# Kernel tuning notes

Hardware: AMD Instinct MI355X
Metric: run time of the kernel (lower is better)

Reference implementation:

```python
import jax, jax.numpy as jnp
import numpy as np

N_HOPS = 3
VOCAB, D = 100000, 300
B, S, T = 128, 2048, 4
N_CLASSES = 3


def setup_inputs() -> dict:
    key = jax.random.key(0)
    ks = jax.random.split(key, 9)
    return {
        "inputs": jax.random.randint(ks[0], (B, S), 0, VOCAB, dtype=jnp.int64 if jax.config.jax_enable_x64 else jnp.int32),
        "targets": jax.random.randint(ks[1], (B, T), 0, VOCAB, dtype=jnp.int64 if jax.config.jax_enable_x64 else jnp.int32),
        "emb_table": jax.random.normal(ks[2], (VOCAB, D), dtype=jnp.float32) * 0.1,
        "W_att": jax.random.normal(ks[3], (2 * D, 1), dtype=jnp.float32) * 0.05,
        "b_att": jax.random.normal(ks[4], (1,), dtype=jnp.float32) * 0.05,
        "W_tr": jax.random.normal(ks[5], (D, D), dtype=jnp.float32) * 0.05,
        "b_tr": jax.random.normal(ks[6], (D,), dtype=jnp.float32) * 0.05,
        "W_out": jax.random.normal(ks[7], (D, N_CLASSES), dtype=jnp.float32) * 0.05,
        "b_out": jax.random.normal(ks[8], (N_CLASSES,), dtype=jnp.float32) * 0.05,
    }


def reference(inputs, targets, emb_table, W_att, b_att, W_tr, b_tr, W_out, b_out):
    # Embedding lookups (dropout prob = 0.0 -> identity)
    we = emb_table[inputs]    # [B, S, D] word/context embeddings
    te = emb_table[targets]   # [B, T, D] aspect-term embeddings
    d = we.shape[-1]
    # Split concat-linear: cat([we, u]) @ W_att == we @ Wa + u @ Wu (avoids [B,S,2D] intermediate)
    Wa, Wu = W_att[:d], W_att[d:]          # each [D, 1]
    u = jnp.mean(te, axis=1, keepdims=True)  # [B, 1, D]
    for _ in range(N_HOPS):
        g = jnp.tanh(we @ Wa + u @ Wu + b_att)          # [B, S, 1]
        a = jax.nn.softmax(g, axis=1)                    # softmax over sequence
        vec = jnp.einsum('bs,bsd->bd', a[..., 0], we)    # [B, D] attention-weighted sum
        te = vec[:, None, :] + te @ W_tr + b_tr          # [B, T, D] (broadcast add)
        u = jnp.mean(te, axis=1, keepdims=True)          # [B, 1, D]
    return u[:, 0, :] @ W_out + b_out                    # [B, n_classes]
```

## Files before the change

### kernel.cpp

```cpp
#include <hip/hip_runtime.h>
#include <hip/hip_bf16.h>

#define VOCAB 100000
#define D 300
#define B 128
#define S 2048
#define T 4

#define WS_V      0
#define WS_WTWU   3600
#define WS_WT2WU  3900
#define WS_WTWO   4200
#define WS_W2WO   5100
#define WS_WT3WO  6000
#define WS_CONST  6900
#define WS_DSCAL  6916
#define WS_PROJ   7940


__device__ __forceinline__ float wave_red(float x) {
    #pragma unroll
    for (int m = 1; m < 64; m <<= 1) x += __shfl_xor(x, m, 64);
    return x;
}

__global__ __launch_bounds__(64) void k_derive1(const float* __restrict__ Watt,
                                                const float* __restrict__ Wtr,
                                                const float* __restrict__ Wout,
                                                float* __restrict__ ws) {
    int i = blockIdx.x, lane = threadIdx.x;
    const float* wrow = Wtr + (size_t)i * D;
    float au = 0.f, a0 = 0.f, a1 = 0.f, a2 = 0.f;
    for (int j = lane; j < D; j += 64) {
        float w = wrow[j];
        au += w * Watt[D + j];
        a0 += w * Wout[j * 3 + 0];
        a1 += w * Wout[j * 3 + 1];
        a2 += w * Wout[j * 3 + 2];
    }
    au = wave_red(au); a0 = wave_red(a0); a1 = wave_red(a1); a2 = wave_red(a2);
    if (lane == 0) {
        ws[WS_WTWU + i] = au;
        ws[WS_WTWO + i * 3 + 0] = a0;
        ws[WS_WTWO + i * 3 + 1] = a1;
        ws[WS_WTWO + i * 3 + 2] = a2;
    }
}

__global__ __launch_bounds__(64) void k_derive2(const float* __restrict__ Wtr,
                                                float* __restrict__ ws) {
    int i = blockIdx.x, lane = threadIdx.x;
    const float* wrow = Wtr + (size_t)i * D;
    float au = 0.f, a0 = 0.f, a1 = 0.f, a2 = 0.f;
    for (int j = lane; j < D; j += 64) {
        float w = wrow[j];
        au += w * ws[WS_WTWU + j];
        a0 += w * ws[WS_WTWO + j * 3 + 0];
        a1 += w * ws[WS_WTWO + j * 3 + 1];
        a2 += w * ws[WS_WTWO + j * 3 + 2];
    }
    au = wave_red(au); a0 = wave_red(a0); a1 = wave_red(a1); a2 = wave_red(a2);
    if (lane == 0) {
        ws[WS_WT2WU + i] = au;
        ws[WS_W2WO + i * 3 + 0] = a0;
        ws[WS_W2WO + i * 3 + 1] = a1;
        ws[WS_W2WO + i * 3 + 2] = a2;
    }
}

__global__ __launch_bounds__(64) void k_derive3(const float* __restrict__ Watt,
                                                const float* __restrict__ Wtr,
                                                const float* __restrict__ Wout,
                                                float* __restrict__ ws) {
    int i = blockIdx.x, lane = threadIdx.x;
    const float* wrow = Wtr + (size_t)i * D;
    float a0 = 0.f, a1 = 0.f, a2 = 0.f;
    for (int j = lane; j < D; j += 64) {
        float w = wrow[j];
        a0 += w * ws[WS_W2WO + j * 3 + 0];
        a1 += w * ws[WS_W2WO + j * 3 + 1];
        a2 += w * ws[WS_W2WO + j * 3 + 2];
    }
    a0 = wave_red(a0); a1 = wave_red(a1); a2 = wave_red(a2);
    if (lane == 0) {
        ws[WS_WT3WO + i * 3 + 0] = a0;
        ws[WS_WT3WO + i * 3 + 1] = a1;
        ws[WS_WT3WO + i * 3 + 2] = a2;
    }
    if (lane < 12) {
        float val;
        if      (lane == 0) val = Watt[i];
        else if (lane == 1) val = Watt[D + i];
        else if (lane == 2) val = ws[WS_WTWU + i];
        else if (lane < 6)  val = Wout[i * 3 + (lane - 3)];
        else if (lane < 9)  val = ws[WS_WTWO + i * 3 + (lane - 6)];
        else                val = ws[WS_W2WO + i * 3 + (lane - 9)];
        ws[WS_V + i * 12 + lane] = val;
    }
}

__global__ __launch_bounds__(64) void k_small(const int* __restrict__ targets,
                                              const float* __restrict__ E,
                                              const float* __restrict__ Watt,
                                              const float* __restrict__ Wout,
                                              const float* __restrict__ btr,
                                              float* __restrict__ ws) {
    int lane = threadIdx.x;
    if (blockIdx.x < B) {
        int b = blockIdx.x;
        int t0 = targets[b * T + 0], t1 = targets[b * T + 1];
        int t2 = targets[b * T + 2], t3 = targets[b * T + 3];
        const float* r0 = E + (size_t)t0 * D;
        const float* r1 = E + (size_t)t1 * D;
        const float* r2 = E + (size_t)t2 * D;
        const float* r3 = E + (size_t)t3 * D;
        float a0 = 0.f, a1 = 0.f, a2 = 0.f, a3 = 0.f, a4 = 0.f, a5 = 0.f;
        for (int i = lane; i < D; i += 64) {
            float u = 0.25f * (r0[i] + r1[i] + r2[i] + r3[i]);
            a0 += u * Watt[D + i];
            a1 += u * ws[WS_WTWU + i];
            a2 += u * ws[WS_WT2WU + i];
            a3 += u * ws[WS_WT3WO + i * 3 + 0];
            a4 += u * ws[WS_WT3WO + i * 3 + 1];
            a5 += u * ws[WS_WT3WO + i * 3 + 2];
        }
        a0 = wave_red(a0); a1 = wave_red(a1); a2 = wave_red(a2);
        a3 = wave_red(a3); a4 = wave_red(a4); a5 = wave_red(a5);
        if (lane == 0) {
            float* o = ws + WS_DSCAL + b * 8;
            o[0] = a0; o[1] = a1; o[2] = a2; o[3] = a3; o[4] = a4; o[5] = a5;
        }
    } else {
        float acc[11];
        #pragma unroll
        for (int k = 0; k < 11; ++k) acc[k] = 0.f;
        for (int i = lane; i < D; i += 64) {
            float bt = btr[i];
            acc[0] += bt * Watt[D + i];
            acc[1] += bt * ws[WS_WTWU + i];
            acc[2] += bt * Wout[i * 3 + 0];
            acc[3] += bt * Wout[i * 3 + 1];
            acc[4] += bt * Wout[i * 3 + 2];
            acc[5] += bt * ws[WS_WTWO + i * 3 + 0];
            acc[6] += bt * ws[WS_WTWO + i * 3 + 1];
            acc[7] += bt * ws[WS_WTWO + i * 3 + 2];
            acc[8] += bt * ws[WS_W2WO + i * 3 + 0];
            acc[9] += bt * ws[WS_W2WO + i * 3 + 1];
            acc[10] += bt * ws[WS_W2WO + i * 3 + 2];
        }
        #pragma unroll
        for (int k = 0; k < 11; ++k) acc[k] = wave_red(acc[k]);
        if (lane == 0) {
            #pragma unroll
            for (int k = 0; k < 11; ++k) ws[WS_CONST + k] = acc[k];
        }
    }
}

__global__ __launch_bounds__(256) void k_proj(const float* __restrict__ E,
                                              const float* __restrict__ Vg,
                                              float* __restrict__ proj) {
    int lane  = threadIdx.x & 63;
    int wave  = (blockIdx.x * blockDim.x + threadIdx.x) >> 6;
    int nwave = (gridDim.x * blockDim.x) >> 6;

    float v[5][12];
    #pragma unroll
    for (int j = 0; j < 5; ++j) {
        int i = lane + 64 * j;
        if (i < D) {
            const float4* p = (const float4*)(Vg + (size_t)i * 12);
            float4 a = p[0], bb = p[1], cc = p[2];
            v[j][0] = a.x;  v[j][1] = a.y;  v[j][2]  = a.z;  v[j][3]  = a.w;
            v[j][4] = bb.x; v[j][5] = bb.y; v[j][6]  = bb.z; v[j][7]  = bb.w;
            v[j][8] = cc.x; v[j][9] = cc.y; v[j][10] = cc.z; v[j][11] = cc.w;
        } else {
            #pragma unroll
            for (int k = 0; k < 12; ++k) v[j][k] = 0.f;
        }
    }

    for (int row = wave; row < VOCAB; row += nwave) {
        const float* er = E + (size_t)row * D;
        float e[5];
        #pragma unroll
        for (int j = 0; j < 5; ++j) {
            int i = lane + 64 * j;
            e[j] = (i < D) ? er[i] : 0.f;
        }
        float p[12];
        #pragma unroll
        for (int k = 0; k < 12; ++k) p[k] = 0.f;
        #pragma unroll
        for (int j = 0; j < 5; ++j) {
            #pragma unroll
            for (int k = 0; k < 12; ++k) p[k] += e[j] * v[j][k];
        }
        #pragma unroll
        for (int m = 1; m < 64; m <<= 1) {
            #pragma unroll
            for (int k = 0; k < 12; ++k) p[k] += __shfl_xor(p[k], m, 64);
        }
        if (lane == 0) {
            float4* dst = (float4*)(proj + (size_t)row * 12);
            dst[0] = make_float4(p[0], p[1], p[2],  p[3]);
            dst[1] = make_float4(p[4], p[5], p[6],  p[7]);
            dst[2] = make_float4(p[8], p[9], p[10], p[11]);
        }
    }
}

__global__ __launch_bounds__(512) void k_hops(const int* __restrict__ inputs,
                                              const float* __restrict__ ws,
                                              const float* __restrict__ batt,
                                              const float* __restrict__ bout,
                                              float* __restrict__ out) {
    __shared__ float wred[8][13];
    __shared__ float sc[4];
    int b = blockIdx.x, tid = threadIdx.x, wave = tid >> 6, lane = tid & 63;
    const float* proj = ws + WS_PROJ;
    const float* cst  = ws + WS_CONST;
    const float* dsc  = ws + WS_DSCAL + b * 8;
    const int*   inp  = inputs + (size_t)b * S;

    float pv[4][12];
    #pragma unroll
    for (int q = 0; q < 4; ++q) {
        int s = tid + 512 * q;
        int idx = inp[s];
        const float4* pr = (const float4*)(proj + (size_t)idx * 12);
        float4 x = pr[0], y = pr[1], z = pr[2];
        pv[q][0] = x.x; pv[q][1] = x.y; pv[q][2]  = x.z; pv[q][3]  = x.w;
        pv[q][4] = y.x; pv[q][5] = y.y; pv[q][6]  = y.z; pv[q][7]  = y.w;
        pv[q][8] = z.x; pv[q][9] = z.y; pv[q][10] = z.z; pv[q][11] = z.w;
    }

    if (tid == 0) sc[0] = dsc[0] + batt[0];
    __syncthreads();
    float c = sc[0];

    float o3c0 = 0.f, o3c1 = 0.f, o3c2 = 0.f, uWtWu = 0.f;

    #pragma unroll
    for (int hop = 0; hop < 3; ++hop) {
        float acc[12];
        #pragma unroll
        for (int k = 0; k < 12; ++k) acc[k] = 0.f;
        #pragma unroll
        for (int q = 0; q < 4; ++q) {
            float g = tanhf(pv[q][0] + c);
            float e = __expf(g);
            acc[11] += e;
            #pragma unroll
            for (int k = 1; k < 12; ++k) acc[k - 1] += e * pv[q][k];
        }
        #pragma unroll
        for (int m = 1; m < 64; m <<= 1) {
            #pragma unroll
            for (int k = 0; k < 12; ++k) acc[k] += __shfl_xor(acc[k], m, 64);
        }
        if (lane == 0) {
            #pragma unroll
            for (int k = 0; k < 12; ++k) wred[wave][k] = acc[k];
        }
        __syncthreads();
        if (tid == 0) {
            float A[12];
            #pragma unroll
            for (int k = 0; k < 12; ++k) {
                float s = 0.f;
                #pragma unroll
                for (int w = 0; w < 8; ++w) s += wred[w][k];
                A[k] = s;
            }
            float inv = 1.0f / A[11];
            if (hop == 0) {
                o3c0  = A[8] * inv + dsc[3] + cst[8];
                o3c1  = A[9] * inv + dsc[4] + cst[9];
                o3c2  = A[10] * inv + dsc[5] + cst[10];
                uWtWu = A[1] * inv + dsc[2] + cst[1];
                sc[0] = A[0] * inv + dsc[1] + cst[0] + batt[0];
            } else if (hop == 1) {
                o3c0  = A[5] * inv + o3c0 + cst[5];
                o3c1  = A[6] * inv + o3c1 + cst[6];
                o3c2  = A[7] * inv + o3c2 + cst[7];
                sc[0] = A[0] * inv + uWtWu + cst[0] + batt[0];
            } else {
                out[b * 3 + 0] = A[2] * inv + o3c0 + cst[2] + bout[0];
                out[b * 3 + 1] = A[3] * inv + o3c1 + cst[3] + bout[1];
                out[b * 3 + 2] = A[4] * inv + o3c2 + cst[4] + bout[2];
            }
        }
        __syncthreads();
        c = sc[0];
    }
}

extern "C" void kernel_launch(void* const* d_in, const int* in_sizes, int n_in,
                              void* d_out, int out_size, void* d_ws, size_t ws_size,
                              hipStream_t stream) {
    const int*   inputs  = (const int*)  d_in[0];
    const int*   targets = (const int*)  d_in[1];
    const float* emb     = (const float*)d_in[2];
    const float* Watt    = (const float*)d_in[3];
    const float* batt    = (const float*)d_in[4];
    const float* Wtr     = (const float*)d_in[5];
    const float* btr     = (const float*)d_in[6];
    const float* Wout    = (const float*)d_in[7];
    const float* bout    = (const float*)d_in[8];
    float* ws  = (float*)d_ws;
    float* out = (float*)d_out;

    hipLaunchKernelGGL(k_derive1, dim3(D),    dim3(64),  0, stream, Watt, Wtr, Wout, ws);
    hipLaunchKernelGGL(k_derive2, dim3(D),    dim3(64),  0, stream, Wtr, ws);
    hipLaunchKernelGGL(k_derive3, dim3(D),    dim3(64),  0, stream, Watt, Wtr, Wout, ws);
    hipLaunchKernelGGL(k_proj,    dim3(2048), dim3(256), 0, stream, emb, ws + WS_V, ws + WS_PROJ);
    hipLaunchKernelGGL(k_small,   dim3(B + 1), dim3(64), 0, stream, targets, emb, Watt, Wout, btr, ws);
    hipLaunchKernelGGL(k_hops,    dim3(B),    dim3(512), 0, stream, inputs, ws, batt, bout, out);
}
```

Baseline: 255.2 us.

## Assign one vocab row per lane in projection and widen hop blocks to 1024

The vocabulary projection kernel now has each lane compute one full embedding row against the 12 projection vectors with float4 loads, instead of one wave per row followed by a 6-step shuffle reduction for 12 values. This removes the per-row cross-lane reduction cost. The trade-off is that adjacent lanes read rows 1200 bytes apart, so loads are strided rather than coalesced. The hop kernel uses 1024 threads per batch row with fewer sequence elements per thread, and the cross-wave sum is parallelised across 12 threads instead of done serially by thread 0.

New measurement: 235.9 us. 7.6% less time.

```diff
diff --git a/kernel.cpp b/kernel.cpp
--- a/kernel.cpp
+++ b/kernel.cpp
@@ -160,62 +160,42 @@
 __global__ __launch_bounds__(256) void k_proj(const float* __restrict__ E,
                                               const float* __restrict__ Vg,
                                               float* __restrict__ proj) {
-    int lane  = threadIdx.x & 63;
-    int wave  = (blockIdx.x * blockDim.x + threadIdx.x) >> 6;
-    int nwave = (gridDim.x * blockDim.x) >> 6;
-
-    float v[5][12];
-    #pragma unroll
-    for (int j = 0; j < 5; ++j) {
-        int i = lane + 64 * j;
-        if (i < D) {
-            const float4* p = (const float4*)(Vg + (size_t)i * 12);
-            float4 a = p[0], bb = p[1], cc = p[2];
-            v[j][0] = a.x;  v[j][1] = a.y;  v[j][2]  = a.z;  v[j][3]  = a.w;
-            v[j][4] = bb.x; v[j][5] = bb.y; v[j][6]  = bb.z; v[j][7]  = bb.w;
-            v[j][8] = cc.x; v[j][9] = cc.y; v[j][10] = cc.z; v[j][11] = cc.w;
-        } else {
-            #pragma unroll
-            for (int k = 0; k < 12; ++k) v[j][k] = 0.f;
-        }
-    }
-
-    for (int row = wave; row < VOCAB; row += nwave) {
-        const float* er = E + (size_t)row * D;
-        float e[5];
-        #pragma unroll
-        for (int j = 0; j < 5; ++j) {
-            int i = lane + 64 * j;
-            e[j] = (i < D) ? er[i] : 0.f;
-        }
-        float p[12];
-        #pragma unroll
-        for (int k = 0; k < 12; ++k) p[k] = 0.f;
-        #pragma unroll
-        for (int j = 0; j < 5; ++j) {
-            #pragma unroll
-            for (int k = 0; k < 12; ++k) p[k] += e[j] * v[j][k];
-        }
-        #pragma unroll
-        for (int m = 1; m < 64; m <<= 1) {
-            #pragma unroll
-            for (int k = 0; k < 12; ++k) p[k] += __shfl_xor(p[k], m, 64);
-        }
-        if (lane == 0) {
-            float4* dst = (float4*)(proj + (size_t)row * 12);
-            dst[0] = make_float4(p[0], p[1], p[2],  p[3]);
-            dst[1] = make_float4(p[4], p[5], p[6],  p[7]);
-            dst[2] = make_float4(p[8], p[9], p[10], p[11]);
-        }
-    }
-}
-
-__global__ __launch_bounds__(512) void k_hops(const int* __restrict__ inputs,
-                                              const float* __restrict__ ws,
-                                              const float* __restrict__ batt,
-                                              const float* __restrict__ bout,
-                                              float* __restrict__ out) {
-    __shared__ float wred[8][13];
+    int lane = threadIdx.x & 63;
+    int wid  = (blockIdx.x * blockDim.x + threadIdx.x) >> 6;
+    int row  = wid * 64 + lane;
+    if (row >= VOCAB) return;
+
+    const float4* er = (const float4*)(E + (size_t)row * D);
+    float acc[12];
+    #pragma unroll
+    for (int c = 0; c < 12; ++c) acc[c] = 0.f;
+
+    #pragma unroll 5
+    for (int k4 = 0; k4 < 75; ++k4) {
+        float4 e = er[k4];
+        const float* vp = Vg + k4 * 48;
+        #pragma unroll
+        for (int c = 0; c < 12; ++c) {
+            acc[c] += e.x * vp[c];
+            acc[c] += e.y * vp[12 + c];
+            acc[c] += e.z * vp[24 + c];
+            acc[c] += e.w * vp[36 + c];
+        }
+    }
+
+    float4* dst = (float4*)(proj + (size_t)row * 12);
+    dst[0] = make_float4(acc[0], acc[1], acc[2],  acc[3]);
+    dst[1] = make_float4(acc[4], acc[5], acc[6],  acc[7]);
+    dst[2] = make_float4(acc[8], acc[9], acc[10], acc[11]);
+}
+
+__global__ __launch_bounds__(1024) void k_hops(const int* __restrict__ inputs,
+                                               const float* __restrict__ ws,
+                                               const float* __restrict__ batt,
+                                               const float* __restrict__ bout,
+                                               float* __restrict__ out) {
+    __shared__ float wred[16][13];
+    __shared__ float Ash[13];
     __shared__ float sc[4];
     int b = blockIdx.x, tid = threadIdx.x, wave = tid >> 6, lane = tid & 63;
     const float* proj = ws + WS_PROJ;
@@ -223,10 +203,10 @@
     const float* dsc  = ws + WS_DSCAL + b * 8;
     const int*   inp  = inputs + (size_t)b * S;
 
-    float pv[4][12];
-    #pragma unroll
-    for (int q = 0; q < 4; ++q) {
-        int s = tid + 512 * q;
+    float pv[2][12];
+    #pragma unroll
+    for (int q = 0; q < 2; ++q) {
+        int s = tid + 1024 * q;
         int idx = inp[s];
         const float4* pr = (const float4*)(proj + (size_t)idx * 12);
         float4 x = pr[0], y = pr[1], z = pr[2];
@@ -247,7 +227,7 @@
         #pragma unroll
         for (int k = 0; k < 12; ++k) acc[k] = 0.f;
         #pragma unroll
-        for (int q = 0; q < 4; ++q) {
+        for (int q = 0; q < 2; ++q) {
             float g = tanhf(pv[q][0] + c);
             float e = __expf(g);
             acc[11] += e;
@@ -264,31 +244,30 @@
             for (int k = 0; k < 12; ++k) wred[wave][k] = acc[k];
         }
         __syncthreads();
+        if (tid < 12) {
+            float s = 0.f;
+            #pragma unroll
+            for (int w = 0; w < 16; ++w) s += wred[w][tid];
+            Ash[tid] = s;
+        }
+        __syncthreads();
         if (tid == 0) {
-            float A[12];
-            #pragma unroll
-            for (int k = 0; k < 12; ++k) {
-                float s = 0.f;
-                #pragma unroll
-                for (int w = 0; w < 8; ++w) s += wred[w][k];
-                A[k] = s;
-            }
-            float inv = 1.0f / A[11];
+            float inv = 1.0f / Ash[11];
             if (hop == 0) {
-                o3c0  = A[8] * inv + dsc[3] + cst[8];
-                o3c1  = A[9] * inv + dsc[4] + cst[9];
-                o3c2  = A[10] * inv + dsc[5] + cst[10];
-                uWtWu = A[1] * inv + dsc[2] + cst[1];
-                sc[0] = A[0] * inv + dsc[1] + cst[0] + batt[0];
+                o3c0  = Ash[8] * inv + dsc[3] + cst[8];
+                o3c1  = Ash[9] * inv + dsc[4] + cst[9];
+                o3c2  = Ash[10] * inv + dsc[5] + cst[10];
+                uWtWu = Ash[1] * inv + dsc[2] + cst[1];
+                sc[0] = Ash[0] * inv + dsc[1] + cst[0] + batt[0];
             } else if (hop == 1) {
-                o3c0  = A[5] * inv + o3c0 + cst[5];
-                o3c1  = A[6] * inv + o3c1 + cst[6];
-                o3c2  = A[7] * inv + o3c2 + cst[7];
-                sc[0] = A[0] * inv + uWtWu + cst[0] + batt[0];
+                o3c0  = Ash[5] * inv + o3c0 + cst[5];
+                o3c1  = Ash[6] * inv + o3c1 + cst[6];
+                o3c2  = Ash[7] * inv + o3c2 + cst[7];
+                sc[0] = Ash[0] * inv + uWtWu + cst[0] + batt[0];
             } else {
-                out[b * 3 + 0] = A[2] * inv + o3c0 + cst[2] + bout[0];
-                out[b * 3 + 1] = A[3] * inv + o3c1 + cst[3] + bout[1];
-                out[b * 3 + 2] = A[4] * inv + o3c2 + cst[4] + bout[2];
+                out[b * 3 + 0] = Ash[2] * inv + o3c0 + cst[2] + bout[0];
+                out[b * 3 + 1] = Ash[3] * inv + o3c1 + cst[3] + bout[1];
+                out[b * 3 + 2] = Ash[4] * inv + o3c2 + cst[4] + bout[2];
             }
         }
         __syncthreads();
@@ -311,10 +290,10 @@
     float* ws  = (float*)d_ws;
     float* out = (float*)d_out;
 
-    hipLaunchKernelGGL(k_derive1, dim3(D),    dim3(64),  0, stream, Watt, Wtr, Wout, ws);
-    hipLaunchKernelGGL(k_derive2, dim3(D),    dim3(64),  0, stream, Wtr, ws);
-    hipLaunchKernelGGL(k_derive3, dim3(D),    dim3(64),  0, stream, Watt, Wtr, Wout, ws);
-    hipLaunchKernelGGL(k_proj,    dim3(2048), dim3(256), 0, stream, emb, ws + WS_V, ws + WS_PROJ);
-    hipLaunchKernelGGL(k_small,   dim3(B + 1), dim3(64), 0, stream, targets, emb, Watt, Wout, btr, ws);
-    hipLaunchKernelGGL(k_hops,    dim3(B),    dim3(512), 0, stream, inputs, ws, batt, bout, out);
-}
+    hipLaunchKernelGGL(k_derive1, dim3(D),    dim3(64),   0, stream, Watt, Wtr, Wout, ws);
+    hipLaunchKernelGGL(k_derive2, dim3(D),    dim3(64),   0, stream, Wtr, ws);
+    hipLaunchKernelGGL(k_derive3, dim3(D),    dim3(64),   0, stream, Watt, Wtr, Wout, ws);
+    hipLaunchKernelGGL(k_proj,    dim3(391),  dim3(256),  0, stream, emb, ws + WS_V, ws + WS_PROJ);
+    hipLaunchKernelGGL(k_small,   dim3(B + 1), dim3(64),  0, stream, targets, emb, Watt, Wout, btr, ws);
+    hipLaunchKernelGGL(k_hops,    dim3(B),    dim3(1024), 0, stream, inputs, ws, batt, bout, out);
+}
```
